# Kernel optimization log

Measured on AMD Instinct MI355X. Metric: run time of the kernel, lower is better.

## Reference

```python
import jax, jax.numpy as jnp
import numpy as np

B, S, D, H = 4, 2048, 1024, 1024  # batch, seq, input_dim, hidden_dim

def setup_inputs() -> dict:
    key = jax.random.key(0)
    k1, k2, k3, k4, k5 = jax.random.split(key, 5)
    scale1 = 1.0 / np.sqrt(D)
    scale2 = 1.0 / np.sqrt(H)
    return {
        "x": jax.random.normal(k1, (B, S, D), dtype=jnp.float32),
        "W1": jax.random.uniform(k2, (D, 3 * H), jnp.float32, -scale1, scale1),
        "b1": jax.random.uniform(k3, (3 * H,), jnp.float32, -scale1, scale1),
        "W2": jax.random.uniform(k4, (H, H), jnp.float32, -scale2, scale2),
        "b2": jax.random.uniform(k5, (H,), jnp.float32, -scale2, scale2),
    }

def reference(x, W1, b1, W2, b2):
    qkv = jnp.einsum('bsd,dh->bsh', x, W1) + b1          # [B,S,3H]
    q, k, v = jnp.split(qkv, 3, axis=-1)                  # each [B,S,H]
    scale = (2.0 * D) ** -0.5                             # faithful: (input_dim*2)^-0.5
    scores = jnp.einsum('bse,bSe->bsS', q, k) * scale     # [B,S,S]
    att = jax.nn.softmax(scores, axis=-1)
    ctx = jnp.einsum('bsS,bSe->bse', att, v)              # [B,S,H]
    out = jnp.einsum('bsh,hk->bsk', ctx, W2) + b2
    return out
```

## Files before the change

kernel.cpp:

```cpp
#include <hip/hip_runtime.h>
#include <hip/hip_bf16.h>
#include <stdint.h>

#define B_  4
#define S_  2048
#define D_  1024
#define H_  1024
#define BS_ (B_*S_)
#define N3H (3*H_)

typedef __bf16 bf16x8 __attribute__((ext_vector_type(8)));
typedef float  f32x4  __attribute__((ext_vector_type(4)));
typedef unsigned short u16x8 __attribute__((ext_vector_type(8)));

__device__ __forceinline__ unsigned short f2bf(float x) {
    unsigned u = __float_as_uint(x);
    return (unsigned short)((u + 0x7FFFu + ((u >> 16) & 1u)) >> 16);
}
__device__ __forceinline__ float bf2f(unsigned short h) {
    return __uint_as_float(((unsigned)h) << 16);
}

__device__ __forceinline__ void gload_lds16(const void* g, void* l) {
    __builtin_amdgcn_global_load_lds(
        (const __attribute__((address_space(1))) void*)g,
        (__attribute__((address_space(3))) void*)l, 16, 0, 0);
}

#define BAR __builtin_amdgcn_s_barrier()
#define DS_FENCE do { asm volatile("s_waitcnt lgkmcnt(0)" ::: "memory"); \
                      __builtin_amdgcn_sched_barrier(0); } while (0)

template<int EPI>
__global__ __launch_bounds__(512, 2) void gemm128(
    const unsigned short* __restrict__ A,
    const unsigned short* __restrict__ Bm,
    int NXt, int NYt, int N, int K,
    long long sAz, long long sBz, long long sOz,
    void* __restrict__ out0, void* __restrict__ out1, void* __restrict__ out2,
    const float* __restrict__ bias, float scale)
{
    __shared__ __align__(16) char lds[3 * 49152];

    const int nt_g = (int)gridDim.x;
    const int bid = (int)blockIdx.x;
    const int C = nt_g >> 3;
    const int c = bid >> 3;
    const int xcd = bid & 7;
    const int qq = c >> 2;
    const int txl = qq % NXt;
    const int rest = (c & 3) + 4 * (qq / NXt);
    const int tile = xcd * C + rest * NXt + txl;
    const int tx = tile % NXt;
    const int rest2 = tile / NXt;
    const int ty = rest2 % NYt;
    const int tz = rest2 / NYt;

    const unsigned short* Ab = A  + (long long)tz * sAz;
    const unsigned short* Bb = Bm + (long long)tz * sBz;
    const int rowBase = ty * 256;
    const int colBase = tx * 128;
    const int tid = threadIdx.x;
    const int w = tid >> 6, l = tid & 63;
    const int wr = w >> 1, wc = w & 1;
    const int fr = l & 15, fq = l >> 4;

    int sr[2], scl[2];
#pragma unroll
    for (int j = 0; j < 2; j++) {
        int o  = j * 8192 + tid * 16;
        int st = o >> 10;
        int wi = o & 1023;
        wi ^= ((wi >> 9) & 1) << 5;
        sr[j]  = (st >> 1) * 16 + (wi >> 6);
        scl[j] = (st & 1) * 32 + ((wi & 63) >> 1);
    }

    auto STAGE_A = [&](char* buf, int half, int t) {
        char* dst = buf + half * 16384 + w * 1024;
        const unsigned short* base =
            Ab + (long long)(rowBase + half * 128) * K + t * 64;
#pragma unroll
        for (int j = 0; j < 2; j++)
            gload_lds16(base + (long long)sr[j] * K + scl[j], dst + j * 8192);
    };
    auto STAGE_B = [&](char* buf, int half, int t) {
        char* dst = buf + 32768 + half * 8192 + w * 1024;
        const unsigned short* base =
            Bb + (long long)(colBase + half * 64) * K + t * 64;
        gload_lds16(base + (long long)sr[0] * K + scl[0], dst);
    };

    const int abase = (fr * 64 + fq * 16) ^ ((fr & 8) << 2);

#define MFMA44(AF, BF, NOFF) do { \
    __builtin_amdgcn_s_setprio(1); \
    _Pragma("unroll") for (int m_ = 0; m_ < 4; m_++) \
    _Pragma("unroll") for (int n_ = 0; n_ < 2; n_++) \
    _Pragma("unroll") for (int k_ = 0; k_ < 2; k_++) \
        acc[m_][(NOFF)+n_] = __builtin_amdgcn_mfma_f32_16x16x32_bf16( \
            AF[m_][k_], BF[n_][k_], acc[m_][(NOFF)+n_], 0, 0, 0); \
    __builtin_amdgcn_s_setprio(0); } while (0)

    f32x4 acc[4][4];
#pragma unroll
    for (int m = 0; m < 4; m++)
#pragma unroll
        for (int n = 0; n < 4; n++) acc[m][n] = (f32x4){0.f, 0.f, 0.f, 0.f};

    const int NT = K >> 6;

    STAGE_A(lds, 0, 0); STAGE_B(lds, 0, 0); STAGE_A(lds, 1, 0); STAGE_B(lds, 1, 0);
    STAGE_A(lds + 49152, 0, 1); STAGE_B(lds + 49152, 0, 1);
    STAGE_A(lds + 49152, 1, 1); STAGE_B(lds + 49152, 1, 1);
    asm volatile("s_waitcnt vmcnt(6)" ::: "memory");
    BAR;
    __builtin_amdgcn_sched_barrier(0);

    bf16x8 afA[4][2], bfA[2][2], bfB[2][2];

    for (int t = 0; t < NT; ++t) {
        const char* bc = lds + (t % 3) * 49152;
        char* bs = lds + ((t + 2) % 3) * 49152;
        int ts = t + 2; if (ts >= NT) ts -= NT;
        const char* Abw = bc + (wr >> 1) * 16384 + (wr & 1) * 8192;
        const char* Bbw = bc + 32768 + wc * 8192;

#pragma unroll
        for (int m = 0; m < 4; m++)
#pragma unroll
            for (int kk = 0; kk < 2; kk++)
                afA[m][kk] = *(const bf16x8*)(Abw + m * 2048 + kk * 1024 + abase);
#pragma unroll
        for (int n = 0; n < 2; n++)
#pragma unroll
            for (int kk = 0; kk < 2; kk++)
                bfA[n][kk] = *(const bf16x8*)(Bbw + n * 2048 + kk * 1024 + abase);
        STAGE_A(bs, 0, ts); STAGE_B(bs, 0, ts);
        BAR; DS_FENCE;
        MFMA44(afA, bfA, 0);
        BAR;

#pragma unroll
        for (int n = 0; n < 2; n++)
#pragma unroll
            for (int kk = 0; kk < 2; kk++)
                bfB[n][kk] = *(const bf16x8*)(Bbw + (n + 2) * 2048 + kk * 1024 + abase);
        STAGE_A(bs, 1, ts); STAGE_B(bs, 1, ts);
        BAR; DS_FENCE;
        MFMA44(afA, bfB, 2);
        asm volatile("s_waitcnt vmcnt(6)" ::: "memory");
        BAR;
        __builtin_amdgcn_sched_barrier(0);
    }

    asm volatile("s_waitcnt vmcnt(0) lgkmcnt(0)" ::: "memory");

    const int crow0 = rowBase + wr * 64 + fq * 4;
    const int ccol0 = colBase + wc * 64 + fr;

#pragma unroll
    for (int n = 0; n < 4; n++) {
        const int col = ccol0 + n * 16;
        if constexpr (EPI == 0) {
            const float bv = bias[col];
            const int seg = col >> 10, scn = col & 1023;
            unsigned short* dst =
                (unsigned short*)(seg == 0 ? out0 : (seg == 1 ? out1 : out2));
#pragma unroll
            for (int m = 0; m < 4; m++) {
                const int r0 = crow0 + m * 16;
#pragma unroll
                for (int j = 0; j < 4; j++)
                    dst[(long long)(r0 + j) * 1024 + scn] = f2bf(acc[m][n][j] + bv);
            }
        } else if constexpr (EPI == 1) {
            unsigned short* dst = (unsigned short*)out0 + (long long)tz * sOz;
#pragma unroll
            for (int m = 0; m < 4; m++) {
                const int r0 = crow0 + m * 16;
#pragma unroll
                for (int j = 0; j < 4; j++)
                    dst[(long long)(r0 + j) * N + col] = f2bf(acc[m][n][j] * scale);
            }
        } else {
            float* dst = (float*)out0;
            const float bv = bias[col];
#pragma unroll
            for (int m = 0; m < 4; m++) {
                const int r0 = crow0 + m * 16;
#pragma unroll
                for (int j = 0; j < 4; j++)
                    dst[(long long)(r0 + j) * N + col] = acc[m][n][j] + bv;
            }
        }
    }
#undef MFMA44
}

template<int EPI>
__global__ __launch_bounds__(512, 2) void gemm256(
    const unsigned short* __restrict__ A,
    const unsigned short* __restrict__ Bm,
    int M, int N, int K,
    long long sAz, long long sBz, long long sOz,
    void* __restrict__ out0, void* __restrict__ out1, void* __restrict__ out2,
    const float* __restrict__ bias, float scale)
{
    __shared__ __align__(16) char lds[131072];
    (void)M;

    const unsigned short* Ab = A  + blockIdx.z * sAz;
    const unsigned short* Bb = Bm + blockIdx.z * sBz;
    const int rowBase = blockIdx.y * 256;
    const int colBase = blockIdx.x * 256;
    const int tid = threadIdx.x;
    const int w = tid >> 6, l = tid & 63;
    const int wr = w >> 2, wc = w & 3;
    const int fr = l & 15, fq = l >> 4;

    int sr[2], scl[2];
#pragma unroll
    for (int j = 0; j < 2; j++) {
        int o  = j * 8192 + tid * 16;
        int st = o >> 10;
        int wi = o & 1023;
        wi ^= ((wi >> 9) & 1) << 5;
        sr[j]  = (st >> 1) * 16 + (wi >> 6);
        scl[j] = (st & 1) * 32 + ((wi & 63) >> 1);
    }

    auto STAGE = [&](int buf, int which, int tile) {
        const unsigned short* mat = (which < 2) ? Ab : Bb;
        const int rt0 = ((which < 2) ? rowBase : colBase) + (which & 1) * 128;
        char* dst = lds + buf * 65536 + (which >> 1) * 32768
                        + (which & 1) * 16384 + w * 1024;
        const int k0 = tile * 64;
#pragma unroll
        for (int j = 0; j < 2; j++) {
            const unsigned short* src =
                mat + (long long)(rt0 + sr[j]) * K + k0 + scl[j];
            gload_lds16(src, dst + j * 8192);
        }
    };

    const int abase = (fr * 64 + fq * 16) ^ ((fr & 8) << 2);
    const char* Ah[2] = { lds + wr * 16384, lds + 65536 + wr * 16384 };
    const char* Bh[2] = { lds + 32768 + (wc >> 1) * 16384,
                          lds + 98304 + (wc >> 1) * 16384 };
    const int bn0 = (wc & 1) * 8192;

#define LA(b, m, kk) (*(const bf16x8*)(Ah[b] + (m)*2048 + (kk)*1024 + abase))
#define LB(b, n, kk) (*(const bf16x8*)(Bh[b] + bn0 + (n)*2048 + (kk)*1024 + abase))
#define MFMA16(AF, BF, MOFF, NOFF) do { \
    __builtin_amdgcn_s_setprio(1); \
    _Pragma("unroll") for (int m_ = 0; m_ < 4; m_++) \
    _Pragma("unroll") for (int n_ = 0; n_ < 2; n_++) \
    _Pragma("unroll") for (int k_ = 0; k_ < 2; k_++) \
        acc[(MOFF)+m_][(NOFF)+n_] = __builtin_amdgcn_mfma_f32_16x16x32_bf16( \
            AF[m_][k_], BF[n_][k_], acc[(MOFF)+m_][(NOFF)+n_], 0, 0, 0); \
    __builtin_amdgcn_s_setprio(0); } while (0)

    f32x4 acc[8][4];
#pragma unroll
    for (int m = 0; m < 8; m++)
#pragma unroll
        for (int n = 0; n < 4; n++) acc[m][n] = (f32x4){0.f, 0.f, 0.f, 0.f};

    const int NT = K >> 6;

    STAGE(0, 0, 0); STAGE(0, 1, 0); STAGE(0, 2, 0); STAGE(0, 3, 0);
    STAGE(1, 0, 1); STAGE(1, 1, 1);
    asm volatile("s_waitcnt vmcnt(4)" ::: "memory");
    BAR;
    __builtin_amdgcn_sched_barrier(0);

    bf16x8 afA[4][2], afB[4][2], bfA[2][2], bfB[2][2];

    for (int i = 0; i < NT / 2; i++) {
        const int t1 = 2 * i + 1;
        int t2 = 2 * i + 2; if (t2 >= NT) t2 -= NT;
        int t3 = 2 * i + 3; if (t3 >= NT) t3 -= NT;

#pragma unroll
        for (int m = 0; m < 4; m++) { afA[m][0] = LA(0, m, 0); afA[m][1] = LA(0, m, 1); }
#pragma unroll
        for (int n = 0; n < 2; n++) { bfA[n][0] = LB(0, n, 0); bfA[n][1] = LB(0, n, 1); }
        STAGE(1, 2, t1);
        BAR; DS_FENCE;
        MFMA16(afA, bfA, 0, 0);
        BAR;
#pragma unroll
        for (int m = 0; m < 4; m++) { afB[m][0] = LA(0, 4 + m, 0); afB[m][1] = LA(0, 4 + m, 1); }
        STAGE(1, 3, t1);
        BAR; DS_FENCE;
        MFMA16(afB, bfA, 4, 0);
        BAR;
#pragma unroll
        for (int n = 0; n < 2; n++) { bfB[n][0] = LB(0, 2 + n, 0); bfB[n][1] = LB(0, 2 + n, 1); }
        STAGE(0, 0, t2);
        BAR; DS_FENCE;
        MFMA16(afA, bfB, 0, 2);
        BAR;
        STAGE(0, 1, t2);
        BAR;
        MFMA16(afB, bfB, 4, 2);
        asm volatile("s_waitcnt vmcnt(4)" ::: "memory");
        BAR;
        __builtin_amdgcn_sched_barrier(0);

#pragma unroll
        for (int m = 0; m < 4; m++) { afA[m][0] = LA(1, m, 0); afA[m][1] = LA(1, m, 1); }
#pragma unroll
        for (int n = 0; n < 2; n++) { bfA[n][0] = LB(1, n, 0); bfA[n][1] = LB(1, n, 1); }
        STAGE(0, 2, t2);
        BAR; DS_FENCE;
        MFMA16(afA, bfA, 0, 0);
        BAR;
#pragma unroll
        for (int m = 0; m < 4; m++) { afB[m][0] = LA(1, 4 + m, 0); afB[m][1] = LA(1, 4 + m, 1); }
        STAGE(0, 3, t2);
        BAR; DS_FENCE;
        MFMA16(afB, bfA, 4, 0);
        BAR;
#pragma unroll
        for (int n = 0; n < 2; n++) { bfB[n][0] = LB(1, 2 + n, 0); bfB[n][1] = LB(1, 2 + n, 1); }
        STAGE(1, 0, t3);
        BAR; DS_FENCE;
        MFMA16(afA, bfB, 0, 2);
        BAR;
        STAGE(1, 1, t3);
        BAR;
        MFMA16(afB, bfB, 4, 2);
        asm volatile("s_waitcnt vmcnt(4)" ::: "memory");
        BAR;
        __builtin_amdgcn_sched_barrier(0);
    }

    asm volatile("s_waitcnt vmcnt(0) lgkmcnt(0)" ::: "memory");

    const int crow0 = rowBase + wr * 128 + fq * 4;
    const int ccol0 = colBase + wc * 64 + fr;

#pragma unroll
    for (int n = 0; n < 4; n++) {
        const int col = ccol0 + n * 16;
        if constexpr (EPI == 1) {
            unsigned short* dst = (unsigned short*)out0 + blockIdx.z * sOz;
#pragma unroll
            for (int m = 0; m < 8; m++) {
                const int r0 = crow0 + m * 16;
#pragma unroll
                for (int j = 0; j < 4; j++)
                    dst[(long long)(r0 + j) * N + col] = f2bf(acc[m][n][j] * scale);
            }
        }
    }
    (void)out1; (void)out2; (void)bias;
#undef LA
#undef LB
#undef MFMA16
}

__global__ __launch_bounds__(256) void conv_f32_bf16(
    const float* __restrict__ in, unsigned short* __restrict__ out, int n8)
{
    for (int i = blockIdx.x * blockDim.x + threadIdx.x; i < n8;
         i += gridDim.x * blockDim.x) {
        const float4 a = ((const float4*)in)[2 * i];
        const float4 b = ((const float4*)in)[2 * i + 1];
        u16x8 o;
        o[0] = f2bf(a.x); o[1] = f2bf(a.y); o[2] = f2bf(a.z); o[3] = f2bf(a.w);
        o[4] = f2bf(b.x); o[5] = f2bf(b.y); o[6] = f2bf(b.z); o[7] = f2bf(b.w);
        ((u16x8*)out)[i] = o;
    }
}

__global__ __launch_bounds__(256) void tconv_f32_bf16(
    const float* __restrict__ in, unsigned short* __restrict__ out,
    int rows, int cols)
{
    __shared__ float t[32][33];
    const int c0 = blockIdx.x * 32, r0 = blockIdx.y * 32;
    const int tx = threadIdx.x & 31, ty = threadIdx.x >> 5;
#pragma unroll
    for (int i = 0; i < 4; i++)
        t[ty + 8 * i][tx] = in[(long long)(r0 + ty + 8 * i) * cols + c0 + tx];
    __syncthreads();
#pragma unroll
    for (int i = 0; i < 4; i++)
        out[(long long)(c0 + ty + 8 * i) * rows + r0 + tx] = f2bf(t[tx][ty + 8 * i]);
}

__global__ __launch_bounds__(256) void t_bf16(
    const unsigned short* __restrict__ in, unsigned short* __restrict__ out,
    int rows, int cols, long long sIz, long long sOz)
{
    __shared__ unsigned short t[32][33];
    in  += blockIdx.z * sIz;
    out += blockIdx.z * sOz;
    const int c0 = blockIdx.x * 32, r0 = blockIdx.y * 32;
    const int tx = threadIdx.x & 31, ty = threadIdx.x >> 5;
#pragma unroll
    for (int i = 0; i < 4; i++)
        t[ty + 8 * i][tx] = in[(long long)(r0 + ty + 8 * i) * cols + c0 + tx];
    __syncthreads();
#pragma unroll
    for (int i = 0; i < 4; i++)
        out[(long long)(c0 + ty + 8 * i) * rows + r0 + tx] = t[tx][ty + 8 * i];
}

__global__ __launch_bounds__(256) void softmax_rows(unsigned short* __restrict__ sc)
{
    const long long row = blockIdx.x;
    unsigned short* p = sc + row * S_;
    const int tid = threadIdx.x, w = tid >> 6, l = tid & 63;

    u16x8 v = *reinterpret_cast<const u16x8*>(&p[tid * 8]);
    float f[8];
#pragma unroll
    for (int i = 0; i < 8; i++) f[i] = bf2f(v[i]);

    float m = f[0];
#pragma unroll
    for (int i = 1; i < 8; i++) m = fmaxf(m, f[i]);
    for (int o = 32; o; o >>= 1) m = fmaxf(m, __shfl_xor(m, o));
    __shared__ float red[8];
    if (l == 0) red[w] = m;
    __syncthreads();
    m = fmaxf(fmaxf(red[0], red[1]), fmaxf(red[2], red[3]));

    float s = 0.f;
#pragma unroll
    for (int i = 0; i < 8; i++) { f[i] = __expf(f[i] - m); s += f[i]; }
    for (int o = 32; o; o >>= 1) s += __shfl_xor(s, o);
    if (l == 0) red[4 + w] = s;
    __syncthreads();
    s = red[4] + red[5] + red[6] + red[7];

    const float inv = 1.0f / s;
    u16x8 o8;
#pragma unroll
    for (int i = 0; i < 8; i++) o8[i] = f2bf(f[i] * inv);
    *reinterpret_cast<u16x8*>(&p[tid * 8]) = o8;
}

extern "C" void kernel_launch(void* const* d_in, const int* in_sizes, int n_in,
                              void* d_out, int out_size, void* d_ws, size_t ws_size,
                              hipStream_t stream)
{
    (void)in_sizes; (void)n_in; (void)out_size; (void)ws_size;
    const float* x  = (const float*)d_in[0];
    const float* W1 = (const float*)d_in[1];
    const float* b1 = (const float*)d_in[2];
    const float* W2 = (const float*)d_in[3];
    const float* b2 = (const float*)d_in[4];
    float* out = (float*)d_out;

    char* ws = (char*)d_ws;
    size_t off = 0;
    auto alloc = [&](size_t bytes) {
        void* p = ws + off;
        off += (bytes + 255) & ~(size_t)255;
        return p;
    };
    unsigned short* xbf = (unsigned short*)alloc((size_t)BS_ * D_ * 2);
    unsigned short* w1t = (unsigned short*)alloc((size_t)N3H * D_ * 2);
    unsigned short* w2t = (unsigned short*)alloc((size_t)H_ * H_ * 2);
    unsigned short* q   = (unsigned short*)alloc((size_t)BS_ * H_ * 2);
    unsigned short* k   = (unsigned short*)alloc((size_t)BS_ * H_ * 2);
    unsigned short* v   = (unsigned short*)alloc((size_t)BS_ * H_ * 2);
    unsigned short* vt  = (unsigned short*)alloc((size_t)BS_ * H_ * 2);
    unsigned short* sc  = (unsigned short*)alloc((size_t)B_ * S_ * S_ * 2);
    unsigned short* ctx = v;

    const float scale = 0.022097086912079608f;

    conv_f32_bf16<<<dim3(2048), dim3(256), 0, stream>>>(x, xbf, BS_ * D_ / 8);
    tconv_f32_bf16<<<dim3(N3H / 32, D_ / 32), dim3(256), 0, stream>>>(W1, w1t, D_, N3H);
    tconv_f32_bf16<<<dim3(H_ / 32, H_ / 32), dim3(256), 0, stream>>>(W2, w2t, H_, H_);

    gemm128<0><<<dim3(768), dim3(512), 0, stream>>>(
        xbf, w1t, 24, 32, N3H, D_, 0LL, 0LL, 0LL, q, k, v, b1, 1.0f);

    t_bf16<<<dim3(H_ / 32, S_ / 32, B_), dim3(256), 0, stream>>>(
        v, vt, S_, H_, (long long)S_ * H_, (long long)S_ * H_);

    gemm256<1><<<dim3(S_ / 256, S_ / 256, B_), dim3(512), 0, stream>>>(
        q, k, S_, S_, H_, (long long)S_ * H_, (long long)S_ * H_, (long long)S_ * S_,
        sc, nullptr, nullptr, nullptr, scale);

    softmax_rows<<<dim3(BS_), dim3(256), 0, stream>>>(sc);

    gemm128<1><<<dim3(256), dim3(512), 0, stream>>>(
        sc, vt, 8, 8, H_, S_, (long long)S_ * S_, (long long)H_ * S_,
        (long long)S_ * H_, ctx, nullptr, nullptr, nullptr, 1.0f);

    gemm128<3><<<dim3(256), dim3(512), 0, stream>>>(
        ctx, w2t, 8, 32, H_, H_, 0LL, 0LL, 0LL, out, nullptr, nullptr, b2, 1.0f);
}
```

Before: 206.4 us.

## Split GEMM k-tile into four phases with finer LDS reads and staging

The main-loop body of the templated GEMM now runs four phases per 64-wide k-tile instead of two. Each phase loads one 32-wide k-slice of fragments, issues a single staging load and runs eight MFMAs. This cuts register pressure from fragment arrays and spreads global-to-LDS staging more evenly across the compute. In exchange it adds two more workgroup barriers per iteration and exposes more LDS read latency between smaller MFMA bursts.

```diff
diff --git a/kernel.cpp b/kernel.cpp
--- a/kernel.cpp
+++ b/kernel.cpp
@@ -93,13 +93,12 @@
 
     const int abase = (fr * 64 + fq * 16) ^ ((fr & 8) << 2);
 
-#define MFMA44(AF, BF, NOFF) do { \
+#define MFMA8(AF, BF, NOFF) do { \
     __builtin_amdgcn_s_setprio(1); \
     _Pragma("unroll") for (int m_ = 0; m_ < 4; m_++) \
     _Pragma("unroll") for (int n_ = 0; n_ < 2; n_++) \
-    _Pragma("unroll") for (int k_ = 0; k_ < 2; k_++) \
         acc[m_][(NOFF)+n_] = __builtin_amdgcn_mfma_f32_16x16x32_bf16( \
-            AF[m_][k_], BF[n_][k_], acc[m_][(NOFF)+n_], 0, 0, 0); \
+            AF[m_], BF[n_], acc[m_][(NOFF)+n_], 0, 0, 0); \
     __builtin_amdgcn_s_setprio(0); } while (0)
 
     f32x4 acc[4][4];
@@ -117,7 +116,7 @@
     BAR;
     __builtin_amdgcn_sched_barrier(0);
 
-    bf16x8 afA[4][2], bfA[2][2], bfB[2][2];
+    bf16x8 a0[4], a1[4], b0[2], b1[2];
 
     for (int t = 0; t < NT; ++t) {
         const char* bc = lds + (t % 3) * 49152;
@@ -128,27 +127,40 @@
 
 #pragma unroll
         for (int m = 0; m < 4; m++)
-#pragma unroll
-            for (int kk = 0; kk < 2; kk++)
-                afA[m][kk] = *(const bf16x8*)(Abw + m * 2048 + kk * 1024 + abase);
+            a0[m] = *(const bf16x8*)(Abw + m * 2048 + abase);
 #pragma unroll
         for (int n = 0; n < 2; n++)
-#pragma unroll
-            for (int kk = 0; kk < 2; kk++)
-                bfA[n][kk] = *(const bf16x8*)(Bbw + n * 2048 + kk * 1024 + abase);
-        STAGE_A(bs, 0, ts); STAGE_B(bs, 0, ts);
-        BAR; DS_FENCE;
-        MFMA44(afA, bfA, 0);
+            b0[n] = *(const bf16x8*)(Bbw + n * 2048 + abase);
+        STAGE_A(bs, 0, ts);
+        BAR; DS_FENCE;
+        MFMA8(a0, b0, 0);
         BAR;
 
 #pragma unroll
         for (int n = 0; n < 2; n++)
-#pragma unroll
-            for (int kk = 0; kk < 2; kk++)
-                bfB[n][kk] = *(const bf16x8*)(Bbw + (n + 2) * 2048 + kk * 1024 + abase);
-        STAGE_A(bs, 1, ts); STAGE_B(bs, 1, ts);
-        BAR; DS_FENCE;
-        MFMA44(afA, bfB, 2);
+            b1[n] = *(const bf16x8*)(Bbw + (n + 2) * 2048 + abase);
+        STAGE_A(bs, 1, ts);
+        BAR; DS_FENCE;
+        MFMA8(a0, b1, 2);
+        BAR;
+
+#pragma unroll
+        for (int m = 0; m < 4; m++)
+            a1[m] = *(const bf16x8*)(Abw + m * 2048 + 1024 + abase);
+#pragma unroll
+        for (int n = 0; n < 2; n++)
+            b0[n] = *(const bf16x8*)(Bbw + n * 2048 + 1024 + abase);
+        STAGE_B(bs, 0, ts);
+        BAR; DS_FENCE;
+        MFMA8(a1, b0, 0);
+        BAR;
+
+#pragma unroll
+        for (int n = 0; n < 2; n++)
+            b1[n] = *(const bf16x8*)(Bbw + (n + 2) * 2048 + 1024 + abase);
+        STAGE_B(bs, 1, ts);
+        BAR; DS_FENCE;
+        MFMA8(a1, b1, 2);
         asm volatile("s_waitcnt vmcnt(6)" ::: "memory");
         BAR;
         __builtin_amdgcn_sched_barrier(0);
@@ -195,7 +207,7 @@
             }
         }
     }
-#undef MFMA44
+#undef MFMA8
 }
 
 template<int EPI>
```

Measured after the change: 207.7 us. No clear change (+0.6%).

## Shrink gemm tile to 128x128 with 4 waves, BK=32 and three blocks per CU

Applied to the files above, without the earlier changes.

Replaces the 256x128-tile, 8-wave GEMM kernel (64-wide K steps, split into two halves) with a 128x128-tile, 4-wave kernel that uses 32-wide K steps and a 48KB triple-buffered LDS ring, allowing three blocks per CU. Grid sizes for the QKV projection, attention-times-V, and output projection GEMMs double accordingly. The intent is to improve occupancy and wave-count balance across CUs and to simplify the inner loop to a single barrier phase per K step. The trade-off is lower arithmetic intensity per block, more global loads per FLOP, and twice as many K iterations and barriers.

```diff
diff --git a/kernel.cpp b/kernel.cpp
--- a/kernel.cpp
+++ b/kernel.cpp
@@ -32,7 +32,7 @@
                       __builtin_amdgcn_sched_barrier(0); } while (0)
 
 template<int EPI>
-__global__ __launch_bounds__(512, 2) void gemm128(
+__global__ __launch_bounds__(256, 3) void gemm3b(
     const unsigned short* __restrict__ A,
     const unsigned short* __restrict__ Bm,
     int NXt, int NYt, int N, int K,
@@ -40,7 +40,7 @@
     void* __restrict__ out0, void* __restrict__ out1, void* __restrict__ out2,
     const float* __restrict__ bias, float scale)
 {
-    __shared__ __align__(16) char lds[3 * 49152];
+    __shared__ __align__(16) char lds[3 * 16384];
 
     const int nt_g = (int)gridDim.x;
     const int bid = (int)blockIdx.x;
@@ -58,7 +58,7 @@
 
     const unsigned short* Ab = A  + (long long)tz * sAz;
     const unsigned short* Bb = Bm + (long long)tz * sBz;
-    const int rowBase = ty * 256;
+    const int rowBase = ty * 128;
     const int colBase = tx * 128;
     const int tid = threadIdx.x;
     const int w = tid >> 6, l = tid & 63;
@@ -68,88 +68,69 @@
     int sr[2], scl[2];
 #pragma unroll
     for (int j = 0; j < 2; j++) {
-        int o  = j * 8192 + tid * 16;
+        int o  = j * 4096 + tid * 16;
         int st = o >> 10;
         int wi = o & 1023;
         wi ^= ((wi >> 9) & 1) << 5;
-        sr[j]  = (st >> 1) * 16 + (wi >> 6);
-        scl[j] = (st & 1) * 32 + ((wi & 63) >> 1);
-    }
-
-    auto STAGE_A = [&](char* buf, int half, int t) {
-        char* dst = buf + half * 16384 + w * 1024;
-        const unsigned short* base =
-            Ab + (long long)(rowBase + half * 128) * K + t * 64;
+        sr[j]  = st * 16 + (wi >> 6);
+        scl[j] = (wi & 63) >> 1;
+    }
+
+    auto STAGE_A = [&](char* buf, int t) {
+        const unsigned short* base = Ab + (long long)rowBase * K + t * 32;
 #pragma unroll
         for (int j = 0; j < 2; j++)
-            gload_lds16(base + (long long)sr[j] * K + scl[j], dst + j * 8192);
+            gload_lds16(base + (long long)sr[j] * K + scl[j],
+                        buf + j * 4096 + w * 1024);
     };
-    auto STAGE_B = [&](char* buf, int half, int t) {
-        char* dst = buf + 32768 + half * 8192 + w * 1024;
-        const unsigned short* base =
-            Bb + (long long)(colBase + half * 64) * K + t * 64;
-        gload_lds16(base + (long long)sr[0] * K + scl[0], dst);
+    auto STAGE_B = [&](char* buf, int t) {
+        const unsigned short* base = Bb + (long long)colBase * K + t * 32;
+#pragma unroll
+        for (int j = 0; j < 2; j++)
+            gload_lds16(base + (long long)sr[j] * K + scl[j],
+                        buf + 8192 + j * 4096 + w * 1024);
     };
 
     const int abase = (fr * 64 + fq * 16) ^ ((fr & 8) << 2);
 
-#define MFMA44(AF, BF, NOFF) do { \
-    __builtin_amdgcn_s_setprio(1); \
-    _Pragma("unroll") for (int m_ = 0; m_ < 4; m_++) \
-    _Pragma("unroll") for (int n_ = 0; n_ < 2; n_++) \
-    _Pragma("unroll") for (int k_ = 0; k_ < 2; k_++) \
-        acc[m_][(NOFF)+n_] = __builtin_amdgcn_mfma_f32_16x16x32_bf16( \
-            AF[m_][k_], BF[n_][k_], acc[m_][(NOFF)+n_], 0, 0, 0); \
-    __builtin_amdgcn_s_setprio(0); } while (0)
-
     f32x4 acc[4][4];
 #pragma unroll
     for (int m = 0; m < 4; m++)
 #pragma unroll
         for (int n = 0; n < 4; n++) acc[m][n] = (f32x4){0.f, 0.f, 0.f, 0.f};
 
-    const int NT = K >> 6;
-
-    STAGE_A(lds, 0, 0); STAGE_B(lds, 0, 0); STAGE_A(lds, 1, 0); STAGE_B(lds, 1, 0);
-    STAGE_A(lds + 49152, 0, 1); STAGE_B(lds + 49152, 0, 1);
-    STAGE_A(lds + 49152, 1, 1); STAGE_B(lds + 49152, 1, 1);
-    asm volatile("s_waitcnt vmcnt(6)" ::: "memory");
+    const int NT = K >> 5;
+
+    STAGE_A(lds, 0); STAGE_B(lds, 0);
+    STAGE_A(lds + 16384, 1); STAGE_B(lds + 16384, 1);
+    asm volatile("s_waitcnt vmcnt(4)" ::: "memory");
     BAR;
     __builtin_amdgcn_sched_barrier(0);
 
-    bf16x8 afA[4][2], bfA[2][2], bfB[2][2];
+    bf16x8 af[4], bf[4];
 
     for (int t = 0; t < NT; ++t) {
-        const char* bc = lds + (t % 3) * 49152;
-        char* bs = lds + ((t + 2) % 3) * 49152;
+        const char* bc = lds + (t % 3) * 16384;
+        char* bs = lds + ((t + 2) % 3) * 16384;
         int ts = t + 2; if (ts >= NT) ts -= NT;
-        const char* Abw = bc + (wr >> 1) * 16384 + (wr & 1) * 8192;
-        const char* Bbw = bc + 32768 + wc * 8192;
 
 #pragma unroll
         for (int m = 0; m < 4; m++)
-#pragma unroll
-            for (int kk = 0; kk < 2; kk++)
-                afA[m][kk] = *(const bf16x8*)(Abw + m * 2048 + kk * 1024 + abase);
-#pragma unroll
-        for (int n = 0; n < 2; n++)
-#pragma unroll
-            for (int kk = 0; kk < 2; kk++)
-                bfA[n][kk] = *(const bf16x8*)(Bbw + n * 2048 + kk * 1024 + abase);
-        STAGE_A(bs, 0, ts); STAGE_B(bs, 0, ts);
-        BAR; DS_FENCE;
-        MFMA44(afA, bfA, 0);
-        BAR;
-
-#pragma unroll
-        for (int n = 0; n < 2; n++)
-#pragma unroll
-            for (int kk = 0; kk < 2; kk++)
-                bfB[n][kk] = *(const bf16x8*)(Bbw + (n + 2) * 2048 + kk * 1024 + abase);
-        STAGE_A(bs, 1, ts); STAGE_B(bs, 1, ts);
-        BAR; DS_FENCE;
-        MFMA44(afA, bfB, 2);
-        asm volatile("s_waitcnt vmcnt(6)" ::: "memory");
+            af[m] = *(const bf16x8*)(bc + (wr * 4 + m) * 1024 + abase);
+#pragma unroll
+        for (int n = 0; n < 4; n++)
+            bf[n] = *(const bf16x8*)(bc + 8192 + (wc * 4 + n) * 1024 + abase);
+        STAGE_A(bs, ts); STAGE_B(bs, ts);
+        BAR; DS_FENCE;
+        __builtin_amdgcn_s_setprio(1);
+#pragma unroll
+        for (int m = 0; m < 4; m++)
+#pragma unroll
+            for (int n = 0; n < 4; n++)
+                acc[m][n] = __builtin_amdgcn_mfma_f32_16x16x32_bf16(
+                    af[m], bf[n], acc[m][n], 0, 0, 0);
+        __builtin_amdgcn_s_setprio(0);
+        asm volatile("s_waitcnt vmcnt(4)" ::: "memory");
         BAR;
         __builtin_amdgcn_sched_barrier(0);
     }
@@ -195,7 +176,6 @@
             }
         }
     }
-#undef MFMA44
 }
 
 template<int EPI>
@@ -480,8 +460,8 @@
     tconv_f32_bf16<<<dim3(N3H / 32, D_ / 32), dim3(256), 0, stream>>>(W1, w1t, D_, N3H);
     tconv_f32_bf16<<<dim3(H_ / 32, H_ / 32), dim3(256), 0, stream>>>(W2, w2t, H_, H_);
 
-    gemm128<0><<<dim3(768), dim3(512), 0, stream>>>(
-        xbf, w1t, 24, 32, N3H, D_, 0LL, 0LL, 0LL, q, k, v, b1, 1.0f);
+    gemm3b<0><<<dim3(1536), dim3(256), 0, stream>>>(
+        xbf, w1t, 24, 64, N3H, D_, 0LL, 0LL, 0LL, q, k, v, b1, 1.0f);
 
     t_bf16<<<dim3(H_ / 32, S_ / 32, B_), dim3(256), 0, stream>>>(
         v, vt, S_, H_, (long long)S_ * H_, (long long)S_ * H_);
@@ -492,10 +472,10 @@
 
     softmax_rows<<<dim3(BS_), dim3(256), 0, stream>>>(sc);
 
-    gemm128<1><<<dim3(256), dim3(512), 0, stream>>>(
-        sc, vt, 8, 8, H_, S_, (long long)S_ * S_, (long long)H_ * S_,
+    gemm3b<1><<<dim3(512), dim3(256), 0, stream>>>(
+        sc, vt, 8, 16, H_, S_, (long long)S_ * S_, (long long)H_ * S_,
         (long long)S_ * H_, ctx, nullptr, nullptr, nullptr, 1.0f);
 
-    gemm128<3><<<dim3(256), dim3(512), 0, stream>>>(
-        ctx, w2t, 8, 32, H_, H_, 0LL, 0LL, 0LL, out, nullptr, nullptr, b2, 1.0f);
-}
+    gemm3b<3><<<dim3(512), dim3(256), 0, stream>>>(
+        ctx, w2t, 8, 64, H_, H_, 0LL, 0LL, 0LL, out, nullptr, nullptr, b2, 1.0f);
+}
```

Measured after the change: 213.7 us. 1.04x slower.
